# Performance work log

Measured on AMD Instinct MI355X. Metric: run time of the kernel, lower is better.

## Reference

```python
import jax, jax.numpy as jnp
import numpy as np

N = 50000
DIM = 768   # input_dim == feature dim (self.L)
D_ATT = 128 # self.D


def setup_inputs() -> dict:
    key = jax.random.key(0)
    ks = jax.random.split(key, 6)
    s = lambda fan_in: 1.0 / np.sqrt(fan_in)
    return {
        "x": jax.random.normal(ks[0], (1, N, DIM), dtype=jnp.float32),
        "W_feat": jax.random.normal(ks[1], (DIM, DIM), dtype=jnp.float32) * s(DIM),
        "b_feat": jax.random.normal(ks[2], (DIM,), dtype=jnp.float32) * s(DIM),
        "W_a": jax.random.normal(ks[3], (D_ATT, DIM), dtype=jnp.float32) * s(DIM),
        "W_b": jax.random.normal(ks[4], (D_ATT, DIM), dtype=jnp.float32) * s(DIM),
        "W_c": jax.random.normal(ks[5], (1, D_ATT), dtype=jnp.float32) * s(D_ATT),
    }


def reference(x, W_feat, b_feat, W_a, W_b, W_c):
    # x: [1, N, DIM] -> squeeze bag dim -> [N, DIM]
    h = jax.nn.relu(jnp.einsum('nd,ed->ne', x[0], W_feat) + b_feat)  # [N, 768]
    a = jax.nn.relu(jnp.einsum('nd,kd->nk', h, W_a))      # [N, 128]
    b = jax.nn.sigmoid(jnp.einsum('nd,kd->nk', h, W_b))   # [N, 128]
    logits = jnp.einsum('nk,ok->on', a * b, W_c)           # [1, N] (transpose fused)
    A = jax.nn.softmax(logits, axis=-1)                    # [1, N]
    return jnp.einsum('on,nd->od', A, h)                   # [1, 768]
```

## Files before the change

kernel.cpp:

```cpp
#include <hip/hip_runtime.h>
#include <hip/hip_bf16.h>
#include <stdint.h>

#define DEVINL __device__ __forceinline__

using bf16x8 = __attribute__((ext_vector_type(8))) short;
using f32x4  = __attribute__((ext_vector_type(4))) float;

static constexpr int NPTS = 50000;
static constexpr int NPAD = 50176;
static constexpr int DIM  = 768;
static constexpr int DATT = 128;
static constexpr int NRB  = NPAD / 128;
static constexpr int NSMB = 49;

DEVINL ushort f2b(float f) {
  uint32_t u = __float_as_uint(f);
  u += 0x7fffu + ((u >> 16) & 1u);
  return (ushort)(u >> 16);
}
DEVINL float b2f(ushort u) { return __uint_as_float(((uint32_t)u) << 16); }

DEVINL void gload_lds16(const void* g, void* l) {
  __builtin_amdgcn_global_load_lds((const __attribute__((address_space(1))) void*)g,
                                   (__attribute__((address_space(3))) void*)l,
                                   16, 0, 0);
}

__global__ void cvt8_kernel(const float* __restrict__ src, ushort* __restrict__ dst,
                            int n8_src, int n8_dst) {
  const int stride = gridDim.x * blockDim.x;
  for (int i = blockIdx.x * blockDim.x + threadIdx.x; i < n8_dst; i += stride) {
    float4 v0 = {0.f, 0.f, 0.f, 0.f}, v1 = {0.f, 0.f, 0.f, 0.f};
    if (i < n8_src) {
      const float4* s4 = (const float4*)src;
      v0 = s4[(long)i * 2];
      v1 = s4[(long)i * 2 + 1];
    }
    ushort4 o0 = { f2b(v0.x), f2b(v0.y), f2b(v0.z), f2b(v0.w) };
    ushort4 o1 = { f2b(v1.x), f2b(v1.y), f2b(v1.z), f2b(v1.w) };
    ((ushort4*)dst)[(long)i * 2]     = o0;
    ((ushort4*)dst)[(long)i * 2 + 1] = o1;
  }
}

__global__ void cvt_weights_kernel(const float* __restrict__ Wf, const float* __restrict__ Wa,
                                   const float* __restrict__ Wb,
                                   ushort* __restrict__ wfb, ushort* __restrict__ wab,
                                   ushort* __restrict__ wbb) {
  const int NF = DIM * DIM / 8, NA = DATT * DIM / 8;
  int i = blockIdx.x * blockDim.x + threadIdx.x;
  const float* src; ushort* dst; int j;
  if (i < NF)               { src = Wf; dst = wfb; j = i; }
  else if (i < NF + NA)     { src = Wa; dst = wab; j = i - NF; }
  else if (i < NF + 2 * NA) { src = Wb; dst = wbb; j = i - NF - NA; }
  else return;
  const float4* s4 = (const float4*)src;
  float4 v0 = s4[(long)j * 2];
  float4 v1 = s4[(long)j * 2 + 1];
  ushort4 o0 = { f2b(v0.x), f2b(v0.y), f2b(v0.z), f2b(v0.w) };
  ushort4 o1 = { f2b(v1.x), f2b(v1.y), f2b(v1.z), f2b(v1.w) };
  ((ushort4*)dst)[(long)j * 2]     = o0;
  ((ushort4*)dst)[(long)j * 2 + 1] = o1;
}

__global__ __launch_bounds__(512)
void gemm_h_kernel(const ushort* __restrict__ A, const ushort* __restrict__ B,
                   const float* __restrict__ bias, ushort* __restrict__ H) {
  __shared__ __align__(16) char lds[4][32768];

  const int tid  = threadIdx.x;
  const int wid  = tid >> 6;
  const int lane = tid & 63;

  const int bid = blockIdx.x;
  const int xcd = bid & 7, idx = bid >> 3;
  const int wgid = (xcd < 4 ? xcd * 74 : 4 * 74 + (xcd - 4) * 73) + idx;
  const int row0 = (wgid / 3) * 256;
  const int col0 = (wgid % 3) * 256;

  const ushort* Abase = A + (long)row0 * DIM;
  const ushort* Bbase = B + (long)col0 * DIM;

  const int pre = (lane & 7) ^ (lane >> 3);
  const int sr0 = wid * 16 + ((lane >> 3) << 1) + (pre >> 2);
  const int sc0 = (pre & 3) * 8;

  auto STAGE_A = [&](int tt) {
    const int buf = tt & 3;
    const long k0 = (long)tt * 32;
#pragma unroll
    for (int i = 0; i < 2; ++i)
      gload_lds16(Abase + (long)(i * 128 + sr0) * DIM + k0 + sc0,
                  &lds[buf][(i * 64 + wid * 8) * 128]);
  };
  auto STAGE_B = [&](int tt) {
    const int buf = tt & 3;
    const long k0 = (long)tt * 32;
#pragma unroll
    for (int i = 0; i < 2; ++i)
      gload_lds16(Bbase + (long)(i * 128 + sr0) * DIM + k0 + sc0,
                  &lds[buf][16384 + (i * 64 + wid * 8) * 128]);
  };

  f32x4 acc0[4][4] = {};
  f32x4 acc1[4][4] = {};

  const int wrbase = (wid >> 2) * 128;
  const int wcbase = (wid & 3) * 64;

  auto PHASE = [&](int t, int ch, f32x4 (&ac)[4][4]) {
    const int buf = t & 3;
    const ushort* Ab = (const ushort*)&lds[buf][0];
    const ushort* Bb = (const ushort*)&lds[buf][16384];
    const int j = lane >> 4;
    bf16x8 a[4], b[4];
#pragma unroll
    for (int fm = 0; fm < 4; ++fm) {
      const int ra = wrbase + ch * 64 + fm * 16 + (lane & 15);
      const int pr = ra >> 1;
      const int sl = (j + 4 * (ra & 1)) ^ (pr & 7);
      a[fm] = *(const bf16x8*)(Ab + pr * 64 + sl * 8);
    }
#pragma unroll
    for (int fn = 0; fn < 4; ++fn) {
      const int rb = wcbase + fn * 16 + (lane & 15);
      const int pr = rb >> 1;
      const int sl = (j + 4 * (rb & 1)) ^ (pr & 7);
      b[fn] = *(const bf16x8*)(Bb + pr * 64 + sl * 8);
    }
    if (t < 22) { if (ch == 0) STAGE_A(t + 2); else STAGE_B(t + 2); }
    __builtin_amdgcn_sched_barrier(0);
    __builtin_amdgcn_s_setprio(1);
#pragma unroll
    for (int fn = 0; fn < 4; ++fn)
#pragma unroll
      for (int fm = 0; fm < 4; ++fm)
        ac[fm][fn] = __builtin_amdgcn_mfma_f32_16x16x32_bf16(a[fm], b[fn], ac[fm][fn], 0, 0, 0);
    __builtin_amdgcn_s_setprio(0);
    __builtin_amdgcn_sched_barrier(0);
  };

  STAGE_A(0); STAGE_B(0); STAGE_A(1); STAGE_B(1);

#pragma unroll 1
  for (int t = 0; t < 24; ++t) {
    if (t < 23) asm volatile("s_waitcnt vmcnt(4)" ::: "memory");
    else        asm volatile("s_waitcnt vmcnt(0)" ::: "memory");
    __builtin_amdgcn_s_barrier();
    PHASE(t, 0, acc0);
    if (t < 23) asm volatile("s_waitcnt vmcnt(4)" ::: "memory");
    else        asm volatile("s_waitcnt vmcnt(0)" ::: "memory");
    __builtin_amdgcn_s_barrier();
    PHASE(t, 1, acc1);
  }

  const int lq = lane >> 4;
  const int lc = lane & 15;
#pragma unroll
  for (int fn = 0; fn < 4; ++fn) {
    const int cg = col0 + wcbase + fn * 16 + lc;
    const float bv = bias[cg];
#pragma unroll
    for (int fm = 0; fm < 4; ++fm) {
      const int rg0 = row0 + wrbase + fm * 16 + lq * 4;
#pragma unroll
      for (int r2 = 0; r2 < 4; ++r2) {
        float v0 = acc0[fm][fn][r2] + bv;
        H[(long)(rg0 + r2) * DIM + cg] = f2b(fmaxf(v0, 0.0f));
        float v1 = acc1[fm][fn][r2] + bv;
        H[(long)(rg0 + 64 + r2) * DIM + cg] = f2b(fmaxf(v1, 0.0f));
      }
    }
  }
}

__global__ __launch_bounds__(512)
void gate_kernel(const ushort* __restrict__ Hm, const ushort* __restrict__ Wa,
                 const ushort* __restrict__ Wb, const float* __restrict__ Wc,
                 float* __restrict__ logits) {
  __shared__ ushort Hs [128 * 64];
  __shared__ ushort Was[128 * 64];
  __shared__ ushort Wbs[128 * 64];
  const int tid  = threadIdx.x;
  const int wid  = tid >> 6;
  const int lane = tid & 63;
  const int row0 = blockIdx.x * 128;

  f32x4 fa[8] = {};
  f32x4 fb[8] = {};

  const int ld_r = lane >> 3;
  const int ld_c = (lane & 7) * 8;

  for (int k0 = 0; k0 < DIM; k0 += 64) {
    __syncthreads();
#pragma unroll
    for (int i = 0; i < 2; ++i) {
      const int ch = i * 8 + wid;
      const int r  = ch * 8 + ld_r;
      gload_lds16(Hm + (long)(row0 + r) * DIM + k0 + ld_c, Hs  + ch * 512);
      gload_lds16(Wa + (long)r * DIM        + k0 + ld_c, Was + ch * 512);
      gload_lds16(Wb + (long)r * DIM        + k0 + ld_c, Wbs + ch * 512);
    }
    __syncthreads();
#pragma unroll
    for (int kk = 0; kk < 2; ++kk) {
      const int kc = kk * 32 + (lane >> 4) * 8;
      bf16x8 h = *(const bf16x8*)(Hs + (wid * 16 + (lane & 15)) * 64 + kc);
#pragma unroll
      for (int n = 0; n < 8; ++n) {
        bf16x8 wa = *(const bf16x8*)(Was + (n * 16 + (lane & 15)) * 64 + kc);
        bf16x8 wb = *(const bf16x8*)(Wbs + (n * 16 + (lane & 15)) * 64 + kc);
        fa[n] = __builtin_amdgcn_mfma_f32_16x16x32_bf16(h, wa, fa[n], 0, 0, 0);
        fb[n] = __builtin_amdgcn_mfma_f32_16x16x32_bf16(h, wb, fb[n], 0, 0, 0);
      }
    }
  }

  const int lc = lane & 15;
  const int lq = lane >> 4;
  float g[4];
#pragma unroll
  for (int r = 0; r < 4; ++r) {
    float s = 0.f;
#pragma unroll
    for (int n = 0; n < 8; ++n) {
      float av = fmaxf(fa[n][r], 0.f);
      float sg = 1.f / (1.f + expf(-fb[n][r]));
      s += av * sg * Wc[n * 16 + lc];
    }
    s += __shfl_xor(s, 1);
    s += __shfl_xor(s, 2);
    s += __shfl_xor(s, 4);
    s += __shfl_xor(s, 8);
    g[r] = s;
  }
  if (lc == 0) {
    const int rbase = row0 + wid * 16 + lq * 4;
#pragma unroll
    for (int r = 0; r < 4; ++r) {
      const int nidx = rbase + r;
      if (nidx < NPTS) logits[nidx] = g[r];
    }
  }
}

__global__ __launch_bounds__(1024)
void softmax_part_kernel(const float* __restrict__ logits, float* __restrict__ part2) {
  __shared__ float red[1024];
  const int tid = threadIdx.x;
  const int n = blockIdx.x * 1024 + tid;
  const float v = (n < NPTS) ? logits[n] : -1e30f;
  red[tid] = v; __syncthreads();
  for (int s = 512; s > 0; s >>= 1) {
    if (tid < s) red[tid] = fmaxf(red[tid], red[tid + s]);
    __syncthreads();
  }
  const float m = red[0];
  __syncthreads();
  red[tid] = (n < NPTS) ? expf(v - m) : 0.f;
  __syncthreads();
  for (int s = 512; s > 0; s >>= 1) {
    if (tid < s) red[tid] += red[tid + s];
    __syncthreads();
  }
  if (tid == 0) { part2[blockIdx.x * 2] = m; part2[blockIdx.x * 2 + 1] = red[0]; }
}

__global__ void softmax_comb_kernel(const float* __restrict__ part2,
                                    float* __restrict__ stats) {
  const int l = threadIdx.x;
  float m = (l < NSMB) ? part2[l * 2]     : -1e30f;
  float s = (l < NSMB) ? part2[l * 2 + 1] : 0.f;
  float M = m;
  for (int o = 32; o > 0; o >>= 1) M = fmaxf(M, __shfl_xor(M, o));
  float sc = s * expf(m - M);
  for (int o = 32; o > 0; o >>= 1) sc += __shfl_xor(sc, o);
  if (l == 0) { stats[0] = M; stats[1] = sc; }
}

__global__ __launch_bounds__(192)
void weighted_partial_kernel(const ushort* __restrict__ Hm, const float* __restrict__ logits,
                             const float* __restrict__ stats, float* __restrict__ part) {
  __shared__ float w[128];
  const int b = blockIdx.x, tid = threadIdx.x;
  const int n0 = b * 128;
  if (tid < 128) {
    const int n = n0 + tid;
    w[tid] = (n < NPTS) ? expf(logits[n] - stats[0]) : 0.f;
  }
  __syncthreads();
  float4 acc = {0.f, 0.f, 0.f, 0.f};
  const ushort* hp = Hm + (long)n0 * DIM + tid * 4;
#pragma unroll 4
  for (int r = 0; r < 128; ++r) {
    const float wr = w[r];
    ushort4 v = *(const ushort4*)(hp + (long)r * DIM);
    acc.x += wr * b2f(v.x);
    acc.y += wr * b2f(v.y);
    acc.z += wr * b2f(v.z);
    acc.w += wr * b2f(v.w);
  }
  ((float4*)(part + (long)b * DIM))[tid] = acc;
}

__global__ void final_reduce_kernel(const float* __restrict__ part,
                                    const float* __restrict__ stats,
                                    float* __restrict__ out) {
  const int c = blockIdx.x * blockDim.x + threadIdx.x;
  if (c >= DIM) return;
  float s = 0.f;
  for (int b = 0; b < NRB; ++b) s += part[(long)b * DIM + c];
  out[c] = s / stats[1];
}

extern "C" void kernel_launch(void* const* d_in, const int* in_sizes, int n_in,
                              void* d_out, int out_size, void* d_ws, size_t ws_size,
                              hipStream_t stream) {
  const float* x  = (const float*)d_in[0];
  const float* Wf = (const float*)d_in[1];
  const float* bf = (const float*)d_in[2];
  const float* Wa = (const float*)d_in[3];
  const float* Wb = (const float*)d_in[4];
  const float* Wc = (const float*)d_in[5];
  float* out = (float*)d_out;

  char* p = (char*)d_ws;
  ushort* xb  = (ushort*)p; p += (size_t)NPAD * DIM * 2;
  ushort* hb  = (ushort*)p; p += (size_t)NPAD * DIM * 2;
  ushort* wfb = (ushort*)p; p += (size_t)DIM * DIM * 2;
  ushort* wab = (ushort*)p; p += (size_t)DATT * DIM * 2;
  ushort* wbb = (ushort*)p; p += (size_t)DATT * DIM * 2;
  float* logits = (float*)p; p += (size_t)NPAD * 4;
  float* stats  = (float*)p; p += 256;
  float* part2  = (float*)p; p += 1024;
  float* part   = (float*)p; p += (size_t)NRB * DIM * 4;

  cvt8_kernel<<<2048, 256, 0, stream>>>(x, xb, NPTS * DIM / 8, NPAD * DIM / 8);
  cvt_weights_kernel<<<384, 256, 0, stream>>>(Wf, Wa, Wb, wfb, wab, wbb);

  gemm_h_kernel<<<196 * 3, 512, 0, stream>>>(xb, wfb, bf, hb);
  gate_kernel<<<NRB, 512, 0, stream>>>(hb, wab, wbb, Wc, logits);
  softmax_part_kernel<<<NSMB, 1024, 0, stream>>>(logits, part2);
  softmax_comb_kernel<<<1, 64, 0, stream>>>(part2, stats);
  weighted_partial_kernel<<<NRB, 192, 0, stream>>>(hb, logits, stats, part);
  final_reduce_kernel<<<3, 256, 0, stream>>>(part, stats, out);
}
```

Baseline: 227.0 us.

## Restructure H GEMM to double-buffered BK=64 tiles with quarter-phase staging

The 768-wide GEMM that builds H now stages 64-wide K slices into two 64 KB LDS buffers instead of 32-wide slices into four 32 KB buffers, with a new XOR swizzle on rows of 64 elements. Each K tile is consumed in four quarter phases (two M halves times two K sub-steps), and the next tile's A and B loads are issued during the first two phases. The aim is fewer main-loop iterations and less waitcnt/barrier overhead per unit of MFMA work. In exchange it adds more barriers per tile and full vmcnt(0) waits, which reduces how far global loads can run ahead of compute.

```diff
diff --git a/kernel.cpp b/kernel.cpp
--- a/kernel.cpp
+++ b/kernel.cpp
@@ -67,7 +67,7 @@
 __global__ __launch_bounds__(512)
 void gemm_h_kernel(const ushort* __restrict__ A, const ushort* __restrict__ B,
                    const float* __restrict__ bias, ushort* __restrict__ H) {
-  __shared__ __align__(16) char lds[4][32768];
+  __shared__ __align__(16) char lds[2][65536];
 
   const int tid  = threadIdx.x;
   const int wid  = tid >> 6;
@@ -79,97 +79,108 @@
   const int row0 = (wgid / 3) * 256;
   const int col0 = (wgid % 3) * 256;
 
+  const int wrbase = (wid >> 2) * 128;
+  const int wcbase = (wid & 3) * 64;
+
   const ushort* Abase = A + (long)row0 * DIM;
   const ushort* Bbase = B + (long)col0 * DIM;
 
-  const int pre = (lane & 7) ^ (lane >> 3);
-  const int sr0 = wid * 16 + ((lane >> 3) << 1) + (pre >> 2);
-  const int sc0 = (pre & 3) * 8;
-
-  auto STAGE_A = [&](int tt) {
-    const int buf = tt & 3;
-    const long k0 = (long)tt * 32;
-#pragma unroll
-    for (int i = 0; i < 2; ++i)
-      gload_lds16(Abase + (long)(i * 128 + sr0) * DIM + k0 + sc0,
-                  &lds[buf][(i * 64 + wid * 8) * 128]);
+  const int srow = lane >> 3;
+  const int scol = ((lane & 7) ^ (lane >> 3)) * 8;
+
+  auto STAGE_A = [&](int t, int d) {
+    const long k0 = (long)t * 64;
+#pragma unroll
+    for (int i = 0; i < 4; ++i) {
+      const int ch = i * 8 + wid;
+      gload_lds16(Abase + (long)(ch * 8 + srow) * DIM + k0 + scol,
+                  &lds[d][ch * 1024]);
+    }
   };
-  auto STAGE_B = [&](int tt) {
-    const int buf = tt & 3;
-    const long k0 = (long)tt * 32;
-#pragma unroll
-    for (int i = 0; i < 2; ++i)
-      gload_lds16(Bbase + (long)(i * 128 + sr0) * DIM + k0 + sc0,
-                  &lds[buf][16384 + (i * 64 + wid * 8) * 128]);
+  auto STAGE_B = [&](int t, int d) {
+    const long k0 = (long)t * 64;
+#pragma unroll
+    for (int i = 0; i < 4; ++i) {
+      const int ch = i * 8 + wid;
+      gload_lds16(Bbase + (long)(ch * 8 + srow) * DIM + k0 + scol,
+                  &lds[d][32768 + ch * 1024]);
+    }
   };
 
   f32x4 acc0[4][4] = {};
   f32x4 acc1[4][4] = {};
 
-  const int wrbase = (wid >> 2) * 128;
-  const int wcbase = (wid & 3) * 64;
-
-  auto PHASE = [&](int t, int ch, f32x4 (&ac)[4][4]) {
-    const int buf = t & 3;
-    const ushort* Ab = (const ushort*)&lds[buf][0];
-    const ushort* Bb = (const ushort*)&lds[buf][16384];
-    const int j = lane >> 4;
+  auto QPHASE = [&](int d, f32x4 (&ac)[4][4], int mh, int kk,
+                    int stage_sel, int stage_t) {
+    const ushort* Ab = (const ushort*)&lds[d][0];
+    const ushort* Bb = (const ushort*)&lds[d][32768];
+    const int j = kk * 4 + (lane >> 4);
     bf16x8 a[4], b[4];
 #pragma unroll
-    for (int fm = 0; fm < 4; ++fm) {
-      const int ra = wrbase + ch * 64 + fm * 16 + (lane & 15);
-      const int pr = ra >> 1;
-      const int sl = (j + 4 * (ra & 1)) ^ (pr & 7);
-      a[fm] = *(const bf16x8*)(Ab + pr * 64 + sl * 8);
-    }
-#pragma unroll
-    for (int fn = 0; fn < 4; ++fn) {
-      const int rb = wcbase + fn * 16 + (lane & 15);
-      const int pr = rb >> 1;
-      const int sl = (j + 4 * (rb & 1)) ^ (pr & 7);
-      b[fn] = *(const bf16x8*)(Bb + pr * 64 + sl * 8);
-    }
-    if (t < 22) { if (ch == 0) STAGE_A(t + 2); else STAGE_B(t + 2); }
+    for (int m = 0; m < 4; ++m) {
+      const int ra = wrbase + mh * 64 + m * 16 + (lane & 15);
+      a[m] = *(const bf16x8*)(Ab + ra * 64 + ((j ^ (ra & 7)) << 3));
+    }
+#pragma unroll
+    for (int n = 0; n < 4; ++n) {
+      const int rb = wcbase + n * 16 + (lane & 15);
+      b[n] = *(const bf16x8*)(Bb + rb * 64 + ((j ^ (rb & 7)) << 3));
+    }
+    if (stage_sel == 1)      STAGE_A(stage_t, d ^ 1);
+    else if (stage_sel == 2) STAGE_B(stage_t, d ^ 1);
+    asm volatile("s_waitcnt lgkmcnt(0)" ::: "memory");
     __builtin_amdgcn_sched_barrier(0);
     __builtin_amdgcn_s_setprio(1);
 #pragma unroll
-    for (int fn = 0; fn < 4; ++fn)
-#pragma unroll
-      for (int fm = 0; fm < 4; ++fm)
-        ac[fm][fn] = __builtin_amdgcn_mfma_f32_16x16x32_bf16(a[fm], b[fn], ac[fm][fn], 0, 0, 0);
+    for (int n = 0; n < 4; ++n)
+#pragma unroll
+      for (int m = 0; m < 4; ++m)
+        ac[m][n] = __builtin_amdgcn_mfma_f32_16x16x32_bf16(a[m], b[n], ac[m][n], 0, 0, 0);
     __builtin_amdgcn_s_setprio(0);
     __builtin_amdgcn_sched_barrier(0);
   };
 
-  STAGE_A(0); STAGE_B(0); STAGE_A(1); STAGE_B(1);
+  STAGE_A(0, 0); STAGE_B(0, 0);
+  STAGE_A(1, 1); STAGE_B(1, 1);
 
 #pragma unroll 1
-  for (int t = 0; t < 24; ++t) {
-    if (t < 23) asm volatile("s_waitcnt vmcnt(4)" ::: "memory");
-    else        asm volatile("s_waitcnt vmcnt(0)" ::: "memory");
-    __builtin_amdgcn_s_barrier();
-    PHASE(t, 0, acc0);
-    if (t < 23) asm volatile("s_waitcnt vmcnt(4)" ::: "memory");
-    else        asm volatile("s_waitcnt vmcnt(0)" ::: "memory");
-    __builtin_amdgcn_s_barrier();
-    PHASE(t, 1, acc1);
+  for (int it = 0; it < 6; ++it) {
+    const int t0 = it * 2;
+    asm volatile("s_waitcnt vmcnt(0)" ::: "memory");
+    __builtin_amdgcn_s_barrier();
+    QPHASE(0, acc0, 0, 0, (it > 0) ? 1 : 0, t0 + 1);
+    __builtin_amdgcn_s_barrier();
+    QPHASE(0, acc0, 0, 1, (it > 0) ? 2 : 0, t0 + 1);
+    __builtin_amdgcn_s_barrier();
+    QPHASE(0, acc1, 1, 0, 0, 0);
+    __builtin_amdgcn_s_barrier();
+    QPHASE(0, acc1, 1, 1, 0, 0);
+    asm volatile("s_waitcnt vmcnt(0)" ::: "memory");
+    __builtin_amdgcn_s_barrier();
+    QPHASE(1, acc0, 0, 0, (it < 5) ? 1 : 0, t0 + 2);
+    __builtin_amdgcn_s_barrier();
+    QPHASE(1, acc0, 0, 1, (it < 5) ? 2 : 0, t0 + 2);
+    __builtin_amdgcn_s_barrier();
+    QPHASE(1, acc1, 1, 0, 0, 0);
+    __builtin_amdgcn_s_barrier();
+    QPHASE(1, acc1, 1, 1, 0, 0);
   }
 
   const int lq = lane >> 4;
   const int lc = lane & 15;
 #pragma unroll
-  for (int fn = 0; fn < 4; ++fn) {
-    const int cg = col0 + wcbase + fn * 16 + lc;
+  for (int n = 0; n < 4; ++n) {
+    const int cg = col0 + wcbase + n * 16 + lc;
     const float bv = bias[cg];
 #pragma unroll
-    for (int fm = 0; fm < 4; ++fm) {
-      const int rg0 = row0 + wrbase + fm * 16 + lq * 4;
+    for (int m = 0; m < 4; ++m) {
+      const int rg = row0 + wrbase + m * 16 + lq * 4;
 #pragma unroll
       for (int r2 = 0; r2 < 4; ++r2) {
-        float v0 = acc0[fm][fn][r2] + bv;
-        H[(long)(rg0 + r2) * DIM + cg] = f2b(fmaxf(v0, 0.0f));
-        float v1 = acc1[fm][fn][r2] + bv;
-        H[(long)(rg0 + 64 + r2) * DIM + cg] = f2b(fmaxf(v1, 0.0f));
+        float v0 = acc0[m][n][r2] + bv;
+        H[(long)(rg + r2) * DIM + cg] = f2b(fmaxf(v0, 0.0f));
+        float v1 = acc1[m][n][r2] + bv;
+        H[(long)(rg + 64 + r2) * DIM + cg] = f2b(fmaxf(v1, 0.0f));
       }
     }
   }
```

Result: faster. 221.6 us (-2.4%).
